# Kernel tuning notes

Hardware: AMD Instinct MI355X
Metric: run time of the kernel (lower is better)

The kernel has to match this reference:

```python
import jax, jax.numpy as jnp
import numpy as np

B, S = 2, 1024
HIDDEN = 2048
NUM_K, NUM_V = 16, 32
DK, DV = 128, 128
KCONV = 4
EPS = 1e-6
KEY_DIM = NUM_K * DK      # 2048
VAL_DIM = NUM_V * DV      # 4096
RATIO = NUM_V // NUM_K    # 2


def setup_inputs() -> dict:
    key = jax.random.key(0)
    ks = jax.random.split(key, 8)
    sc = lambda k, shape, s=0.02: jax.random.normal(k, shape, jnp.float32) * s
    return {
        "hidden_states": jax.random.normal(ks[0], (B, S, HIDDEN), jnp.float32),
        "W_qkvz": sc(ks[1], (HIDDEN, 2 * KEY_DIM + 2 * VAL_DIM)),
        "W_ba": sc(ks[2], (HIDDEN, 2 * NUM_V)),
        "conv_weight": sc(ks[3], (2 * KEY_DIM + VAL_DIM, KCONV), 0.1),
        "A_log": jnp.log(jax.random.uniform(ks[4], (NUM_V,), jnp.float32, 0.001, 16.0)),
        "dt_bias": jnp.ones((NUM_V,), jnp.float32),
        "norm_weight": jnp.ones((DV,), jnp.float32),
        "W_out": sc(ks[5], (VAL_DIM, HIDDEN)),
    }


def _l2norm(x):
    return x * jax.lax.rsqrt(jnp.sum(x * x, axis=-1, keepdims=True) + 1e-6)


def reference(hidden_states, W_qkvz, W_ba, conv_weight, A_log, dt_bias, norm_weight, W_out):
    Bb, Ss, _ = hidden_states.shape
    # fused in_proj + fix_query_key_value_ordering: per k-head layout [q|k|ratio*v|ratio*z]
    qkvz = (hidden_states @ W_qkvz).reshape(Bb, Ss, NUM_K, 2 * DK + 2 * RATIO * DV)
    q = qkvz[..., :DK]                                        # [B,S,NUM_K,DK]
    k = qkvz[..., DK:2 * DK]
    v = qkvz[..., 2 * DK:2 * DK + RATIO * DV].reshape(Bb, Ss, NUM_V, DV)
    z = qkvz[..., 2 * DK + RATIO * DV:].reshape(Bb, Ss, NUM_V, DV)
    ba = (hidden_states @ W_ba).reshape(Bb, Ss, NUM_K, 2 * RATIO)
    b = ba[..., :RATIO].reshape(Bb, Ss, NUM_V)
    a = ba[..., RATIO:].reshape(Bb, Ss, NUM_V)
    # causal depthwise conv over mixed qkv channels + silu (causal_conv1d)
    mixed = jnp.concatenate(
        [q.reshape(Bb, Ss, -1), k.reshape(Bb, Ss, -1), v.reshape(Bb, Ss, -1)], axis=-1)
    x = jnp.transpose(mixed, (0, 2, 1))                       # [B,C,S]
    x = jnp.pad(x, ((0, 0), (0, 0), (KCONV - 1, 0)))
    conv = jax.lax.conv_general_dilated(
        x, conv_weight[:, None, :], (1,), 'VALID',
        feature_group_count=x.shape[1],
        dimension_numbers=('NCH', 'OIH', 'NCH'))
    mixed = jax.nn.silu(jnp.transpose(conv, (0, 2, 1)))       # [B,S,conv_dim]
    q = mixed[..., :KEY_DIM].reshape(Bb, Ss, NUM_K, DK)
    k = mixed[..., KEY_DIM:2 * KEY_DIM].reshape(Bb, Ss, NUM_K, DK)
    v = mixed[..., 2 * KEY_DIM:].reshape(Bb, Ss, NUM_V, DV)
    # GQA: repeat each k-head to its RATIO consecutive v-heads
    q = jnp.repeat(q, RATIO, axis=2)
    k = jnp.repeat(k, RATIO, axis=2)
    q = _l2norm(q) * (DK ** -0.5)
    k = _l2norm(k)
    # fused_gdn_gating: g = -exp(A_log) * softplus(a + dt_bias); beta = sigmoid(b)
    g = -jnp.exp(A_log) * jax.nn.softplus(a + dt_bias)        # [B,S,H] fp32
    beta = jax.nn.sigmoid(b)
    # recurrent gated delta rule scan; state [B,H,DK,DV]
    def step(state, inp):
        qt, kt, vt, gt, bt = inp
        state = state * jnp.exp(gt)[..., None, None]
        pred = jnp.einsum('bhk,bhkv->bhv', kt, state)
        delta = (vt - pred) * bt[..., None]
        state = state + kt[..., None] * delta[..., None, :]
        out = jnp.einsum('bhk,bhkv->bhv', qt, state)
        return state, out

    xs = (q.transpose(1, 0, 2, 3), k.transpose(1, 0, 2, 3), v.transpose(1, 0, 2, 3),
          g.transpose(1, 0, 2), beta.transpose(1, 0, 2))
    state0 = jnp.zeros((Bb, NUM_V, DK, DV), jnp.float32)
    _, core = jax.lax.scan(step, state0, xs)                  # [S,B,H,DV]
    core = core.transpose(1, 0, 2, 3)
    # RMSNormGated (norm_before_gate=True): rmsnorm(x) * w * silu(z)
    var = jnp.mean(core * core, axis=-1, keepdims=True)
    core = core * jax.lax.rsqrt(var + EPS) * norm_weight * jax.nn.silu(z)
    return core.reshape(Bb, Ss, VAL_DIM) @ W_out              # [B,S,HIDDEN]
```

## Files before the change

### kernel.cpp

```cpp
#include <hip/hip_runtime.h>
#include <stdint.h>

#define B_ 2
#define S_ 1024
#define HID 2048
#define NK 16
#define NV 32
#define DK_ 128
#define DV_ 128
#define QKVZ_N 12288
#define TOK (B_*S_)
#define KROW 144

typedef unsigned short u16;
typedef __bf16 bf16x8 __attribute__((ext_vector_type(8)));
typedef float f32x4 __attribute__((ext_vector_type(4)));
typedef float f32x2 __attribute__((ext_vector_type(2)));
typedef unsigned short u16x8 __attribute__((ext_vector_type(8)));
typedef unsigned short u16x4 __attribute__((ext_vector_type(4)));

__device__ __forceinline__ float bf2f(u16 u) {
    return __builtin_bit_cast(float, (unsigned)u << 16);
}
__device__ __forceinline__ u16 f2bf(float f) {
    unsigned u = __builtin_bit_cast(unsigned, f);
    u += 0x7fff + ((u >> 16) & 1);
    return (u16)(u >> 16);
}

template <int CTRL>
__device__ __forceinline__ float dpp_add(float x) {
    int yi = __builtin_amdgcn_update_dpp(0, __builtin_bit_cast(int, x), CTRL, 0xF, 0xF, true);
    return x + __builtin_bit_cast(float, yi);
}
__device__ __forceinline__ float sum16(float x) {
    x = dpp_add<0xB1>(x);
    x = dpp_add<0x4E>(x);
    x = dpp_add<0x141>(x);
    x = dpp_add<0x140>(x);
    return x;
}

__device__ __forceinline__ void gl16(const void* g, void* l) {
    __builtin_amdgcn_global_load_lds((const __attribute__((address_space(1))) uint32_t*)g,
                                     (__attribute__((address_space(3))) uint32_t*)l, 16, 0, 0);
}
__device__ __forceinline__ void gl4(const void* g, void* l) {
    __builtin_amdgcn_global_load_lds((const __attribute__((address_space(1))) uint32_t*)g,
                                     (__attribute__((address_space(3))) uint32_t*)l, 4, 0, 0);
}

__global__ void k_cvt_bf16(const float* __restrict__ in, u16* __restrict__ out, int n) {
    int i = (blockIdx.x * blockDim.x + threadIdx.x) * 4;
    if (i >= n) return;
    float4 v = *(const float4*)(in + i);
    u16x4 o = { f2bf(v.x), f2bf(v.y), f2bf(v.z), f2bf(v.w) };
    *(u16x4*)(out + i) = o;
}

__global__ void k_transpose(const float* __restrict__ in, u16* __restrict__ out, int R, int C) {
    __shared__ float tile[32][33];
    int c0 = blockIdx.x * 32, r0 = blockIdx.y * 32;
    int tx = threadIdx.x, ty = threadIdx.y;
#pragma unroll
    for (int i = 0; i < 4; i++)
        tile[ty + i * 8][tx] = in[(size_t)(r0 + ty + i * 8) * C + c0 + tx];
    __syncthreads();
#pragma unroll
    for (int i = 0; i < 4; i++)
        out[(size_t)(c0 + ty + i * 8) * R + r0 + tx] = f2bf(tile[tx][ty + i * 8]);
}

template <int OUT_BF16>
__global__ __launch_bounds__(256) void k_gemm(const u16* __restrict__ A, const u16* __restrict__ Bt,
                                              void* __restrict__ Cv, int K, int ldc) {
    __shared__ u16 As[128 * 40];
    __shared__ u16 Bs[128 * 40];
    int tid = threadIdx.x;
    int bm = blockIdx.y, bn = blockIdx.x;
    int wid = tid >> 6, lane = tid & 63;
    int wm = wid >> 1, wn = wid & 1;
    int l15 = lane & 15, lg = lane >> 4;
    int srow = tid >> 2, schunk = (tid & 3) * 8;
    const u16* Ag = A + (size_t)(bm * 128 + srow) * K + schunk;
    const u16* Bg = Bt + (size_t)(bn * 128 + srow) * K + schunk;
    f32x4 acc[4][4] = {};
    for (int k0 = 0; k0 < K; k0 += 32) {
        u16x8 a0 = *(const u16x8*)(Ag + k0);
        u16x8 a1 = *(const u16x8*)(Ag + (size_t)64 * K + k0);
        u16x8 b0 = *(const u16x8*)(Bg + k0);
        u16x8 b1 = *(const u16x8*)(Bg + (size_t)64 * K + k0);
        __syncthreads();
        *(u16x8*)&As[srow * 40 + schunk] = a0;
        *(u16x8*)&As[(srow + 64) * 40 + schunk] = a1;
        *(u16x8*)&Bs[srow * 40 + schunk] = b0;
        *(u16x8*)&Bs[(srow + 64) * 40 + schunk] = b1;
        __syncthreads();
        bf16x8 af[4], bf[4];
#pragma unroll
        for (int mi = 0; mi < 4; mi++)
            af[mi] = __builtin_bit_cast(bf16x8, *(const u16x8*)&As[(wm * 64 + mi * 16 + l15) * 40 + lg * 8]);
#pragma unroll
        for (int ni = 0; ni < 4; ni++)
            bf[ni] = __builtin_bit_cast(bf16x8, *(const u16x8*)&Bs[(wn * 64 + ni * 16 + l15) * 40 + lg * 8]);
#pragma unroll
        for (int mi = 0; mi < 4; mi++)
#pragma unroll
            for (int ni = 0; ni < 4; ni++)
                acc[mi][ni] = __builtin_amdgcn_mfma_f32_16x16x32_bf16(af[mi], bf[ni], acc[mi][ni], 0, 0, 0);
    }
#pragma unroll
    for (int mi = 0; mi < 4; mi++) {
        int gr0 = bm * 128 + wm * 64 + mi * 16 + lg * 4;
#pragma unroll
        for (int ni = 0; ni < 4; ni++) {
            int gc = bn * 128 + wn * 64 + ni * 16 + l15;
#pragma unroll
            for (int r = 0; r < 4; r++) {
                if (OUT_BF16)
                    ((u16*)Cv)[(size_t)(gr0 + r) * ldc + gc] = f2bf(acc[mi][ni][r]);
                else
                    ((float*)Cv)[(size_t)(gr0 + r) * ldc + gc] = acc[mi][ni][r];
            }
        }
    }
}

__global__ void k_ba(const float* __restrict__ hid, const float* __restrict__ Wba, float* __restrict__ ba) {
    int token = blockIdx.x;
    int c = threadIdx.x;
    const float* h = hid + (size_t)token * HID;
    const float* w = Wba + c;
    float acc = 0.f;
    for (int k = 0; k < HID; k += 4) {
        float4 hv = *(const float4*)(h + k);
        acc += hv.x * w[(size_t)k * 64] + hv.y * w[(size_t)(k + 1) * 64] +
               hv.z * w[(size_t)(k + 2) * 64] + hv.w * w[(size_t)(k + 3) * 64];
    }
    ba[(size_t)token * 64 + c] = acc;
}

__global__ __launch_bounds__(256) void k_conv(const u16* __restrict__ qkvz, const float* __restrict__ ba,
                                              const float* __restrict__ cw, const float* __restrict__ A_log,
                                              const float* __restrict__ dt_bias, float* __restrict__ qs,
                                              float* __restrict__ ks, float* __restrict__ vs,
                                              float2* __restrict__ gb2) {
    __shared__ float sm[4096];
    int token = blockIdx.x;
    int b = token >> 10;
    int t = token & (S_ - 1);
    int tid = threadIdx.x;
    const u16* row3 = qkvz + (size_t)token * QKVZ_N;
#pragma unroll
    for (int i = 0; i < 32; i++) {
        int c = tid + i * 256;
        int col;
        if (c < 2048) col = (c >> 7) * 768 + (c & 127);
        else if (c < 4096) col = ((c - 2048) >> 7) * 768 + 128 + (c & 127);
        else {
            int cc = c - 4096;
            col = (cc >> 8) * 768 + 256 + ((cc >> 7) & 1) * 128 + (cc & 127);
        }
        float4 w = *(const float4*)(cw + c * 4);
        float x3 = bf2f(row3[col]);
        float x2 = (t >= 1) ? bf2f(row3[col - QKVZ_N]) : 0.f;
        float x1 = (t >= 2) ? bf2f(row3[col - 2 * QKVZ_N]) : 0.f;
        float x0 = (t >= 3) ? bf2f(row3[col - 3 * QKVZ_N]) : 0.f;
        float s = w.x * x0 + w.y * x1 + w.z * x2 + w.w * x3;
        s = s / (1.f + __expf(-s));
        if (c < 4096) sm[c] = s;
        else {
            int cc = c - 4096;
            int hv = cc >> 7, d = cc & 127;
            vs[((size_t)(b * NV + hv) * S_ + t) * 128 + d] = s;
        }
    }
    __syncthreads();
    int grp = tid >> 3, l8 = tid & 7;
    float vals[16];
    float ss = 0.f;
    const float* sp = sm + grp * 128 + l8 * 16;
#pragma unroll
    for (int i = 0; i < 16; i++) { vals[i] = sp[i]; ss += vals[i] * vals[i]; }
    ss += __shfl_xor(ss, 1); ss += __shfl_xor(ss, 2); ss += __shfl_xor(ss, 4);
    float scale = rsqrtf(ss + 1e-6f);
    if (grp < 16) scale *= 0.08838834764831845f;
    float* op = (grp < 16 ? qs : ks) + ((size_t)(b * NK + (grp & 15)) * S_ + t) * KROW
              + l8 * 16 + (l8 >> 1) * 4;
#pragma unroll
    for (int i = 0; i < 16; i++) op[i] = vals[i] * scale;
    if (tid < 32) {
        int hv = tid;
        float bval = ba[(size_t)token * 64 + (hv >> 1) * 4 + (hv & 1)];
        float aval = ba[(size_t)token * 64 + (hv >> 1) * 4 + 2 + (hv & 1)];
        float x = aval + dt_bias[hv];
        float sp2 = (x > 20.f) ? x : log1pf(__expf(x));
        float eg = __expf(-__expf(A_log[hv]) * sp2);
        float bt = 1.f / (1.f + __expf(-bval));
        gb2[(size_t)(b * NV + hv) * S_ + t] = make_float2(eg, bt);
    }
}

__global__ __launch_bounds__(512) void k_scan(const float* __restrict__ qs, const float* __restrict__ ks,
                                              const float* __restrict__ vs, const float2* __restrict__ gb2,
                                              float* __restrict__ core) {
    __shared__ float kb[2][32 * KROW];
    __shared__ float qb[2][32 * KROW];
    __shared__ float vbf[2][32 * 32];
    __shared__ float2 gbl[2][32];
    int bid = blockIdx.x;
    int bh = bid >> 2, vsp = bid & 3;
    int b = bh >> 5, hv = bh & 31, hk = hv >> 1;
    int tid = threadIdx.x;
    int wid = tid >> 6, lane = tid & 63;
    int vloc = tid >> 4, rq = tid & 15;
    const char* kgb = (const char*)(ks + (size_t)(b * NK + hk) * S_ * KROW);
    const char* qgb = (const char*)(qs + (size_t)(b * NK + hk) * S_ * KROW);
    const char* vgb = (const char*)(vs + ((size_t)(b * NV + hv) * S_) * 128 + vsp * 32);
    const char* ggb = (const char*)(gb2 + (size_t)(b * NV + hv) * S_);
    float* cp = core + ((size_t)(b * NV + hv) * S_) * 128 + vsp * 32 + vloc;
    bool writer = (rq == 0);
    int koff = rq * 8 + (rq >> 2) * 4;

    auto stage = [&](int tile, int buf) {
        const char* kg = kgb + (size_t)tile * 32 * (KROW * 4);
        const char* qg = qgb + (size_t)tile * 32 * (KROW * 4);
        const char* vg = vgb + (size_t)tile * 32 * 512;
        const char* gg = ggb + (size_t)tile * 32 * 8;
        for (int ch = wid; ch < 41; ch += 8) {
            if (ch < 18)
                gl16(kg + ch * 1024 + lane * 16, (char*)&kb[buf][0] + ch * 1024);
            else if (ch < 36)
                gl16(qg + (ch - 18) * 1024 + lane * 16, (char*)&qb[buf][0] + (ch - 18) * 1024);
            else if (ch < 40) {
                int c4 = ch - 36;
                gl16(vg + (size_t)(c4 * 8 + (lane >> 3)) * 512 + (lane & 7) * 16,
                     (char*)&vbf[buf][0] + c4 * 1024);
            } else
                gl4(gg + lane * 4, (char*)&gbl[buf][0]);
        }
    };

    f32x2 st2[4] = {};
    stage(0, 0);
    __syncthreads();
    for (int tile = 0; tile < 32; ++tile) {
        int buf = tile & 1;
        if (tile < 31) stage(tile + 1, buf ^ 1);
        const float* kT = &kb[buf][0];
        const float* qT = &qb[buf][0];
        const float* vT = &vbf[buf][0];
        const float2* gT = &gbl[buf][0];
#pragma unroll
        for (int t = 0; t < 32; ++t) {
            f32x4 kA = *(const f32x4*)(kT + t * KROW + koff);
            f32x4 kB = *(const f32x4*)(kT + t * KROW + koff + 4);
            f32x4 qA = *(const f32x4*)(qT + t * KROW + koff);
            f32x4 qB = *(const f32x4*)(qT + t * KROW + koff + 4);
            float vv = vT[t * 32 + vloc];
            float2 gv = gT[t];
            f32x2 k0 = __builtin_shufflevector(kA, kA, 0, 1);
            f32x2 k1 = __builtin_shufflevector(kA, kA, 2, 3);
            f32x2 k2 = __builtin_shufflevector(kB, kB, 0, 1);
            f32x2 k3 = __builtin_shufflevector(kB, kB, 2, 3);
            f32x2 p0 = k0 * st2[0];
            p0 = __builtin_elementwise_fma(k1, st2[1], p0);
            f32x2 p1 = k2 * st2[2];
            p1 = __builtin_elementwise_fma(k3, st2[3], p1);
            f32x2 ps = p0 + p1;
            float dks = sum16(ps.x + ps.y);
            float eg = gv.x;
            float delta = (vv - eg * dks) * gv.y;
            f32x2 e2 = {eg, eg}, d2 = {delta, delta};
            st2[0] = __builtin_elementwise_fma(st2[0], e2, k0 * d2);
            st2[1] = __builtin_elementwise_fma(st2[1], e2, k1 * d2);
            st2[2] = __builtin_elementwise_fma(st2[2], e2, k2 * d2);
            st2[3] = __builtin_elementwise_fma(st2[3], e2, k3 * d2);
            f32x2 q0 = __builtin_shufflevector(qA, qA, 0, 1);
            f32x2 q1 = __builtin_shufflevector(qA, qA, 2, 3);
            f32x2 q2 = __builtin_shufflevector(qB, qB, 0, 1);
            f32x2 q3 = __builtin_shufflevector(qB, qB, 2, 3);
            f32x2 o0 = q0 * st2[0];
            o0 = __builtin_elementwise_fma(q1, st2[1], o0);
            f32x2 o1 = q2 * st2[2];
            o1 = __builtin_elementwise_fma(q3, st2[3], o1);
            f32x2 os = o0 + o1;
            float dqs = sum16(os.x + os.y);
            if (writer) cp[(size_t)(tile * 32 + t) * 128] = dqs;
        }
        __syncthreads();
    }
}

__global__ __launch_bounds__(256) void k_gate(const float* __restrict__ core, const u16* __restrict__ qkvz,
                                              const float* __restrict__ nw, u16* __restrict__ gated) {
    int token = blockIdx.x, tid = threadIdx.x;
    int b = token >> 10, t = token & (S_ - 1);
    int grp = tid >> 3, l8 = tid & 7;
    const float* cp = core + ((size_t)(b * NV + grp) * S_ + t) * DV_ + l8 * 16;
    float vals[16];
    float ss = 0.f;
#pragma unroll
    for (int i = 0; i < 16; i++) { vals[i] = cp[i]; ss += vals[i] * vals[i]; }
    ss += __shfl_xor(ss, 1); ss += __shfl_xor(ss, 2); ss += __shfl_xor(ss, 4);
    float rms = rsqrtf(ss * (1.0f / DV_) + 1e-6f);
    const u16* zp = qkvz + (size_t)token * QKVZ_N + (grp >> 1) * 768 + 512 + (grp & 1) * 128 + l8 * 16;
    u16* op = gated + ((size_t)token * NV + grp) * DV_ + l8 * 16;
#pragma unroll
    for (int i = 0; i < 16; i++) {
        float z = bf2f(zp[i]);
        float sz = z / (1.f + __expf(-z));
        op[i] = f2bf(vals[i] * rms * nw[l8 * 16 + i] * sz);
    }
}

extern "C" void kernel_launch(void* const* d_in, const int* in_sizes, int n_in,
                              void* d_out, int out_size, void* d_ws, size_t ws_size,
                              hipStream_t stream) {
    const float* hidden = (const float*)d_in[0];
    const float* Wqkvz = (const float*)d_in[1];
    const float* Wba = (const float*)d_in[2];
    const float* convw = (const float*)d_in[3];
    const float* A_log = (const float*)d_in[4];
    const float* dt_bias = (const float*)d_in[5];
    const float* norm_w = (const float*)d_in[6];
    const float* Wout = (const float*)d_in[7];

    char* ws = (char*)d_ws;
    size_t off = 0;
    auto alloc = [&](size_t bytes) -> void* {
        void* p = ws + off;
        off += (bytes + 255) & ~(size_t)255;
        return p;
    };
    u16* hiddenB = (u16*)alloc((size_t)TOK * HID * 2);
    u16* WqT = (u16*)alloc((size_t)QKVZ_N * HID * 2);
    u16* WoT = (u16*)alloc((size_t)HID * 4096 * 2);
    u16* qkvz = (u16*)alloc((size_t)TOK * QKVZ_N * 2);
    float* ba = (float*)alloc((size_t)TOK * 64 * 4);
    float* qs = (float*)alloc((size_t)B_ * NK * S_ * KROW * 4);
    float* ks = (float*)alloc((size_t)B_ * NK * S_ * KROW * 4);
    float* vs = (float*)alloc((size_t)B_ * NV * S_ * 128 * 4);
    float2* gb2 = (float2*)alloc((size_t)B_ * NV * S_ * 8);
    float* core = (float*)alloc((size_t)B_ * NV * S_ * 128 * 4);
    u16* gated = (u16*)alloc((size_t)TOK * 4096 * 2);

    k_cvt_bf16<<<4096, 256, 0, stream>>>(hidden, hiddenB, TOK * HID);
    k_transpose<<<dim3(QKVZ_N / 32, HID / 32), dim3(32, 8), 0, stream>>>(Wqkvz, WqT, HID, QKVZ_N);
    k_transpose<<<dim3(HID / 32, 4096 / 32), dim3(32, 8), 0, stream>>>(Wout, WoT, 4096, HID);
    k_gemm<1><<<dim3(QKVZ_N / 128, TOK / 128), 256, 0, stream>>>(hiddenB, WqT, qkvz, HID, QKVZ_N);
    k_ba<<<TOK, 64, 0, stream>>>(hidden, Wba, ba);
    k_conv<<<TOK, 256, 0, stream>>>(qkvz, ba, convw, A_log, dt_bias, qs, ks, vs, gb2);
    k_scan<<<256, 512, 0, stream>>>(qs, ks, vs, gb2, core);
    k_gate<<<TOK, 256, 0, stream>>>(core, qkvz, norm_w, gated);
    k_gemm<0><<<dim3(HID / 128, TOK / 128), 256, 0, stream>>>(gated, WoT, d_out, 4096, HID);
}
```

Baseline: 647.3 us.

## Repad q/k rows, force packed FMA asm, stage scan outputs in LDS

Changes the padded q/k row layout from 144 to 160 floats, with each 8-float group at a stride of 10 floats, to alter LDS bank mapping for the per-lane 2-float loads in the scan kernel. The producer kernel writes q/k with vector stores to match. The recurrence math now uses inline v_pk_mul_f32/v_pk_fma_f32 asm so packed FP32 instructions are guaranteed. Per-step outputs are buffered in a double-buffered LDS tile and written to global memory as coalesced 2-float stores per tile, instead of scattered single-float stores from one lane in sixteen. The cost is more staging traffic and LDS from the wider padding.

Result: slower. 671.9 us (+3.8%).

```diff
diff --git a/kernel.cpp b/kernel.cpp
--- a/kernel.cpp
+++ b/kernel.cpp
@@ -10,7 +10,7 @@
 #define DV_ 128
 #define QKVZ_N 12288
 #define TOK (B_*S_)
-#define KROW 144
+#define KROW 160
 
 typedef unsigned short u16;
 typedef __bf16 bf16x8 __attribute__((ext_vector_type(8)));
@@ -39,6 +39,17 @@
     x = dpp_add<0x141>(x);
     x = dpp_add<0x140>(x);
     return x;
+}
+
+__device__ __forceinline__ f32x2 pk_mul(f32x2 a, f32x2 b) {
+    f32x2 d;
+    asm("v_pk_mul_f32 %0, %1, %2" : "=v"(d) : "v"(a), "v"(b));
+    return d;
+}
+__device__ __forceinline__ f32x2 pk_fma(f32x2 a, f32x2 b, f32x2 c) {
+    f32x2 d;
+    asm("v_pk_fma_f32 %0, %1, %2, %3" : "=v"(d) : "v"(a), "v"(b), "v"(c));
+    return d;
 }
 
 __device__ __forceinline__ void gl16(const void* g, void* l) {
@@ -185,10 +196,13 @@
     ss += __shfl_xor(ss, 1); ss += __shfl_xor(ss, 2); ss += __shfl_xor(ss, 4);
     float scale = rsqrtf(ss + 1e-6f);
     if (grp < 16) scale *= 0.08838834764831845f;
-    float* op = (grp < 16 ? qs : ks) + ((size_t)(b * NK + (grp & 15)) * S_ + t) * KROW
-              + l8 * 16 + (l8 >> 1) * 4;
-#pragma unroll
-    for (int i = 0; i < 16; i++) op[i] = vals[i] * scale;
+    float* op = (grp < 16 ? qs : ks) + ((size_t)(b * NK + (grp & 15)) * S_ + t) * KROW + 20 * l8;
+    *(float4*)(op)      = make_float4(vals[0]*scale, vals[1]*scale, vals[2]*scale, vals[3]*scale);
+    *(float4*)(op + 4)  = make_float4(vals[4]*scale, vals[5]*scale, vals[6]*scale, vals[7]*scale);
+    *(float2*)(op + 10) = make_float2(vals[8]*scale, vals[9]*scale);
+    *(float2*)(op + 12) = make_float2(vals[10]*scale, vals[11]*scale);
+    *(float2*)(op + 14) = make_float2(vals[12]*scale, vals[13]*scale);
+    *(float2*)(op + 16) = make_float2(vals[14]*scale, vals[15]*scale);
     if (tid < 32) {
         int hv = tid;
         float bval = ba[(size_t)token * 64 + (hv >> 1) * 4 + (hv & 1)];
@@ -208,6 +222,7 @@
     __shared__ float qb[2][32 * KROW];
     __shared__ float vbf[2][32 * 32];
     __shared__ float2 gbl[2][32];
+    __shared__ float outb[2][32 * 32];
     int bid = blockIdx.x;
     int bh = bid >> 2, vsp = bid & 3;
     int b = bh >> 5, hv = bh & 31, hk = hv >> 1;
@@ -218,26 +233,26 @@
     const char* qgb = (const char*)(qs + (size_t)(b * NK + hk) * S_ * KROW);
     const char* vgb = (const char*)(vs + ((size_t)(b * NV + hv) * S_) * 128 + vsp * 32);
     const char* ggb = (const char*)(gb2 + (size_t)(b * NV + hv) * S_);
-    float* cp = core + ((size_t)(b * NV + hv) * S_) * 128 + vsp * 32 + vloc;
+    float* cpb = core + ((size_t)(b * NV + hv) * S_) * 128 + vsp * 32;
     bool writer = (rq == 0);
-    int koff = rq * 8 + (rq >> 2) * 4;
-
-    auto stage = [&](int tile, int buf) {
-        const char* kg = kgb + (size_t)tile * 32 * (KROW * 4);
-        const char* qg = qgb + (size_t)tile * 32 * (KROW * 4);
+    int koff = 10 * rq;
+
+    auto stage = [&](int tile, int bufi) {
+        const char* kg = kgb + (size_t)tile * (32 * KROW * 4);
+        const char* qg = qgb + (size_t)tile * (32 * KROW * 4);
         const char* vg = vgb + (size_t)tile * 32 * 512;
-        const char* gg = ggb + (size_t)tile * 32 * 8;
-        for (int ch = wid; ch < 41; ch += 8) {
-            if (ch < 18)
-                gl16(kg + ch * 1024 + lane * 16, (char*)&kb[buf][0] + ch * 1024);
-            else if (ch < 36)
-                gl16(qg + (ch - 18) * 1024 + lane * 16, (char*)&qb[buf][0] + (ch - 18) * 1024);
-            else if (ch < 40) {
-                int c4 = ch - 36;
+        const char* gg = ggb + (size_t)tile * 256;
+        for (int ch = wid; ch < 45; ch += 8) {
+            if (ch < 20)
+                gl16(kg + ch * 1024 + lane * 16, (char*)&kb[bufi][0] + ch * 1024);
+            else if (ch < 40)
+                gl16(qg + (ch - 20) * 1024 + lane * 16, (char*)&qb[bufi][0] + (ch - 20) * 1024);
+            else if (ch < 44) {
+                int c4 = ch - 40;
                 gl16(vg + (size_t)(c4 * 8 + (lane >> 3)) * 512 + (lane & 7) * 16,
-                     (char*)&vbf[buf][0] + c4 * 1024);
+                     (char*)&vbf[bufi][0] + c4 * 1024);
             } else
-                gl4(gg + lane * 4, (char*)&gbl[buf][0]);
+                gl4(gg + lane * 4, (char*)&gbl[bufi][0]);
         }
     };
 
@@ -251,44 +266,42 @@
         const float* qT = &qb[buf][0];
         const float* vT = &vbf[buf][0];
         const float2* gT = &gbl[buf][0];
+        float* oT = &outb[buf][0];
 #pragma unroll
         for (int t = 0; t < 32; ++t) {
-            f32x4 kA = *(const f32x4*)(kT + t * KROW + koff);
-            f32x4 kB = *(const f32x4*)(kT + t * KROW + koff + 4);
-            f32x4 qA = *(const f32x4*)(qT + t * KROW + koff);
-            f32x4 qB = *(const f32x4*)(qT + t * KROW + koff + 4);
+            const float* kr = kT + t * KROW + koff;
+            const float* qr = qT + t * KROW + koff;
+            f32x2 k0 = *(const f32x2*)(kr);
+            f32x2 k1 = *(const f32x2*)(kr + 2);
+            f32x2 k2 = *(const f32x2*)(kr + 4);
+            f32x2 k3 = *(const f32x2*)(kr + 6);
+            f32x2 q0 = *(const f32x2*)(qr);
+            f32x2 q1 = *(const f32x2*)(qr + 2);
+            f32x2 q2 = *(const f32x2*)(qr + 4);
+            f32x2 q3 = *(const f32x2*)(qr + 6);
             float vv = vT[t * 32 + vloc];
             float2 gv = gT[t];
-            f32x2 k0 = __builtin_shufflevector(kA, kA, 0, 1);
-            f32x2 k1 = __builtin_shufflevector(kA, kA, 2, 3);
-            f32x2 k2 = __builtin_shufflevector(kB, kB, 0, 1);
-            f32x2 k3 = __builtin_shufflevector(kB, kB, 2, 3);
-            f32x2 p0 = k0 * st2[0];
-            p0 = __builtin_elementwise_fma(k1, st2[1], p0);
-            f32x2 p1 = k2 * st2[2];
-            p1 = __builtin_elementwise_fma(k3, st2[3], p1);
-            f32x2 ps = p0 + p1;
-            float dks = sum16(ps.x + ps.y);
-            float eg = gv.x;
-            float delta = (vv - eg * dks) * gv.y;
-            f32x2 e2 = {eg, eg}, d2 = {delta, delta};
-            st2[0] = __builtin_elementwise_fma(st2[0], e2, k0 * d2);
-            st2[1] = __builtin_elementwise_fma(st2[1], e2, k1 * d2);
-            st2[2] = __builtin_elementwise_fma(st2[2], e2, k2 * d2);
-            st2[3] = __builtin_elementwise_fma(st2[3], e2, k3 * d2);
-            f32x2 q0 = __builtin_shufflevector(qA, qA, 0, 1);
-            f32x2 q1 = __builtin_shufflevector(qA, qA, 2, 3);
-            f32x2 q2 = __builtin_shufflevector(qB, qB, 0, 1);
-            f32x2 q3 = __builtin_shufflevector(qB, qB, 2, 3);
-            f32x2 o0 = q0 * st2[0];
-            o0 = __builtin_elementwise_fma(q1, st2[1], o0);
-            f32x2 o1 = q2 * st2[2];
-            o1 = __builtin_elementwise_fma(q3, st2[3], o1);
-            f32x2 os = o0 + o1;
-            float dqs = sum16(os.x + os.y);
-            if (writer) cp[(size_t)(tile * 32 + t) * 128] = dqs;
+            f32x2 pa = pk_fma(k1, st2[1], pk_mul(k0, st2[0]));
+            f32x2 pb = pk_fma(k3, st2[3], pk_mul(k2, st2[2]));
+            float dks = sum16((pa.x + pb.x) + (pa.y + pb.y));
+            float delta = (vv - gv.x * dks) * gv.y;
+            f32x2 e2; e2.x = gv.x; e2.y = gv.x;
+            f32x2 d2; d2.x = delta; d2.y = delta;
+            st2[0] = pk_fma(st2[0], e2, pk_mul(k0, d2));
+            st2[1] = pk_fma(st2[1], e2, pk_mul(k1, d2));
+            st2[2] = pk_fma(st2[2], e2, pk_mul(k2, d2));
+            st2[3] = pk_fma(st2[3], e2, pk_mul(k3, d2));
+            f32x2 oa = pk_fma(q1, st2[1], pk_mul(q0, st2[0]));
+            f32x2 ob = pk_fma(q3, st2[3], pk_mul(q2, st2[2]));
+            float dqs = sum16((oa.x + ob.x) + (oa.y + ob.y));
+            if (writer) oT[t * 32 + vloc] = dqs;
         }
         __syncthreads();
+        {
+            int trow = tid >> 4, c2 = (tid & 15) * 2;
+            f32x2 val = *(const f32x2*)&outb[buf][trow * 32 + c2];
+            *(f32x2*)(cpb + (size_t)(tile * 32 + trow) * 128 + c2) = val;
+        }
     }
 }
 
```

## Use direct global-to-LDS loads in GEMM, repad q/k rows, stage scan outputs

Applied to the files above, without the earlier changes.

The GEMM now loads its A and B tiles straight into unpadded LDS with gl16 direct-to-LDS copies, split by wave, instead of going through registers with padded stores. The q/k row stride changes from 144 to 192 floats with a 12-float-per-lane offset pattern, and the prep kernel writes those rows with float4 stores. The scan kernel collects per-timestep outputs in a double-buffered LDS tile and writes them out as coalesced float2 stores after each tile, replacing scattered single-float global writes. The trade-offs are larger LDS and global footprint for q/k, possible bank conflicts from the unpadded GEMM tiles, and extra LDS traffic in the scan.

New measurement: 612.5 us. -5.4%, faster.

```diff
diff --git a/kernel.cpp b/kernel.cpp
--- a/kernel.cpp
+++ b/kernel.cpp
@@ -10,7 +10,7 @@
 #define DV_ 128
 #define QKVZ_N 12288
 #define TOK (B_*S_)
-#define KROW 144
+#define KROW 192
 
 typedef unsigned short u16;
 typedef __bf16 bf16x8 __attribute__((ext_vector_type(8)));
@@ -74,35 +74,33 @@
 template <int OUT_BF16>
 __global__ __launch_bounds__(256) void k_gemm(const u16* __restrict__ A, const u16* __restrict__ Bt,
                                               void* __restrict__ Cv, int K, int ldc) {
-    __shared__ u16 As[128 * 40];
-    __shared__ u16 Bs[128 * 40];
+    __shared__ u16 As[128 * 32];
+    __shared__ u16 Bs[128 * 32];
     int tid = threadIdx.x;
     int bm = blockIdx.y, bn = blockIdx.x;
     int wid = tid >> 6, lane = tid & 63;
     int wm = wid >> 1, wn = wid & 1;
     int l15 = lane & 15, lg = lane >> 4;
-    int srow = tid >> 2, schunk = (tid & 3) * 8;
-    const u16* Ag = A + (size_t)(bm * 128 + srow) * K + schunk;
-    const u16* Bg = Bt + (size_t)(bn * 128 + srow) * K + schunk;
+    const u16* src0 = (wid >> 1) ? (Bt + (size_t)bn * 128 * K) : (A + (size_t)bm * 128 * K);
+    u16* ldsb = (wid >> 1) ? Bs : As;
+    int cbase = (wid & 1) * 4;
+    int lrow = lane >> 2, lcol = (lane & 3) * 8;
     f32x4 acc[4][4] = {};
     for (int k0 = 0; k0 < K; k0 += 32) {
-        u16x8 a0 = *(const u16x8*)(Ag + k0);
-        u16x8 a1 = *(const u16x8*)(Ag + (size_t)64 * K + k0);
-        u16x8 b0 = *(const u16x8*)(Bg + k0);
-        u16x8 b1 = *(const u16x8*)(Bg + (size_t)64 * K + k0);
-        __syncthreads();
-        *(u16x8*)&As[srow * 40 + schunk] = a0;
-        *(u16x8*)&As[(srow + 64) * 40 + schunk] = a1;
-        *(u16x8*)&Bs[srow * 40 + schunk] = b0;
-        *(u16x8*)&Bs[(srow + 64) * 40 + schunk] = b1;
+        if (k0) __syncthreads();
+#pragma unroll
+        for (int c = 0; c < 4; c++) {
+            int ch = cbase + c;
+            gl16(src0 + (size_t)(16 * ch + lrow) * K + k0 + lcol, (char*)ldsb + ch * 1024);
+        }
         __syncthreads();
         bf16x8 af[4], bf[4];
 #pragma unroll
         for (int mi = 0; mi < 4; mi++)
-            af[mi] = __builtin_bit_cast(bf16x8, *(const u16x8*)&As[(wm * 64 + mi * 16 + l15) * 40 + lg * 8]);
+            af[mi] = __builtin_bit_cast(bf16x8, *(const u16x8*)&As[(wm * 64 + mi * 16 + l15) * 32 + lg * 8]);
 #pragma unroll
         for (int ni = 0; ni < 4; ni++)
-            bf[ni] = __builtin_bit_cast(bf16x8, *(const u16x8*)&Bs[(wn * 64 + ni * 16 + l15) * 40 + lg * 8]);
+            bf[ni] = __builtin_bit_cast(bf16x8, *(const u16x8*)&Bs[(wn * 64 + ni * 16 + l15) * 32 + lg * 8]);
 #pragma unroll
         for (int mi = 0; mi < 4; mi++)
 #pragma unroll
@@ -185,10 +183,11 @@
     ss += __shfl_xor(ss, 1); ss += __shfl_xor(ss, 2); ss += __shfl_xor(ss, 4);
     float scale = rsqrtf(ss + 1e-6f);
     if (grp < 16) scale *= 0.08838834764831845f;
-    float* op = (grp < 16 ? qs : ks) + ((size_t)(b * NK + (grp & 15)) * S_ + t) * KROW
-              + l8 * 16 + (l8 >> 1) * 4;
-#pragma unroll
-    for (int i = 0; i < 16; i++) op[i] = vals[i] * scale;
+    float* op = (grp < 16 ? qs : ks) + ((size_t)(b * NK + (grp & 15)) * S_ + t) * KROW + 24 * l8;
+    *(float4*)(op)      = make_float4(vals[0]*scale, vals[1]*scale, vals[2]*scale, vals[3]*scale);
+    *(float4*)(op + 4)  = make_float4(vals[4]*scale, vals[5]*scale, vals[6]*scale, vals[7]*scale);
+    *(float4*)(op + 12) = make_float4(vals[8]*scale, vals[9]*scale, vals[10]*scale, vals[11]*scale);
+    *(float4*)(op + 16) = make_float4(vals[12]*scale, vals[13]*scale, vals[14]*scale, vals[15]*scale);
     if (tid < 32) {
         int hv = tid;
         float bval = ba[(size_t)token * 64 + (hv >> 1) * 4 + (hv & 1)];
@@ -208,6 +207,7 @@
     __shared__ float qb[2][32 * KROW];
     __shared__ float vbf[2][32 * 32];
     __shared__ float2 gbl[2][32];
+    __shared__ float outb[2][32 * 32];
     int bid = blockIdx.x;
     int bh = bid >> 2, vsp = bid & 3;
     int b = bh >> 5, hv = bh & 31, hk = hv >> 1;
@@ -218,26 +218,26 @@
     const char* qgb = (const char*)(qs + (size_t)(b * NK + hk) * S_ * KROW);
     const char* vgb = (const char*)(vs + ((size_t)(b * NV + hv) * S_) * 128 + vsp * 32);
     const char* ggb = (const char*)(gb2 + (size_t)(b * NV + hv) * S_);
-    float* cp = core + ((size_t)(b * NV + hv) * S_) * 128 + vsp * 32 + vloc;
+    float* cpb = core + ((size_t)(b * NV + hv) * S_) * 128 + vsp * 32;
     bool writer = (rq == 0);
-    int koff = rq * 8 + (rq >> 2) * 4;
-
-    auto stage = [&](int tile, int buf) {
-        const char* kg = kgb + (size_t)tile * 32 * (KROW * 4);
-        const char* qg = qgb + (size_t)tile * 32 * (KROW * 4);
+    int koff = 12 * rq;
+
+    auto stage = [&](int tile, int bufi) {
+        const char* kg = kgb + (size_t)tile * (32 * KROW * 4);
+        const char* qg = qgb + (size_t)tile * (32 * KROW * 4);
         const char* vg = vgb + (size_t)tile * 32 * 512;
-        const char* gg = ggb + (size_t)tile * 32 * 8;
-        for (int ch = wid; ch < 41; ch += 8) {
-            if (ch < 18)
-                gl16(kg + ch * 1024 + lane * 16, (char*)&kb[buf][0] + ch * 1024);
-            else if (ch < 36)
-                gl16(qg + (ch - 18) * 1024 + lane * 16, (char*)&qb[buf][0] + (ch - 18) * 1024);
-            else if (ch < 40) {
-                int c4 = ch - 36;
+        const char* gg = ggb + (size_t)tile * 256;
+        for (int ch = wid; ch < 53; ch += 8) {
+            if (ch < 24)
+                gl16(kg + ch * 1024 + lane * 16, (char*)&kb[bufi][0] + ch * 1024);
+            else if (ch < 48)
+                gl16(qg + (ch - 24) * 1024 + lane * 16, (char*)&qb[bufi][0] + (ch - 24) * 1024);
+            else if (ch < 52) {
+                int c4 = ch - 48;
                 gl16(vg + (size_t)(c4 * 8 + (lane >> 3)) * 512 + (lane & 7) * 16,
-                     (char*)&vbf[buf][0] + c4 * 1024);
+                     (char*)&vbf[bufi][0] + c4 * 1024);
             } else
-                gl4(gg + lane * 4, (char*)&gbl[buf][0]);
+                gl4(gg + lane * 4, (char*)&gbl[bufi][0]);
         }
     };
 
@@ -251,6 +251,7 @@
         const float* qT = &qb[buf][0];
         const float* vT = &vbf[buf][0];
         const float2* gT = &gbl[buf][0];
+        float* oT = &outb[buf][0];
 #pragma unroll
         for (int t = 0; t < 32; ++t) {
             f32x4 kA = *(const f32x4*)(kT + t * KROW + koff);
@@ -263,12 +264,9 @@
             f32x2 k1 = __builtin_shufflevector(kA, kA, 2, 3);
             f32x2 k2 = __builtin_shufflevector(kB, kB, 0, 1);
             f32x2 k3 = __builtin_shufflevector(kB, kB, 2, 3);
-            f32x2 p0 = k0 * st2[0];
-            p0 = __builtin_elementwise_fma(k1, st2[1], p0);
-            f32x2 p1 = k2 * st2[2];
-            p1 = __builtin_elementwise_fma(k3, st2[3], p1);
-            f32x2 ps = p0 + p1;
-            float dks = sum16(ps.x + ps.y);
+            f32x2 pa = __builtin_elementwise_fma(k1, st2[1], k0 * st2[0]);
+            f32x2 pb = __builtin_elementwise_fma(k3, st2[3], k2 * st2[2]);
+            float dks = sum16((pa.x + pb.x) + (pa.y + pb.y));
             float eg = gv.x;
             float delta = (vv - eg * dks) * gv.y;
             f32x2 e2 = {eg, eg}, d2 = {delta, delta};
@@ -280,15 +278,17 @@
             f32x2 q1 = __builtin_shufflevector(qA, qA, 2, 3);
             f32x2 q2 = __builtin_shufflevector(qB, qB, 0, 1);
             f32x2 q3 = __builtin_shufflevector(qB, qB, 2, 3);
-            f32x2 o0 = q0 * st2[0];
-            o0 = __builtin_elementwise_fma(q1, st2[1], o0);
-            f32x2 o1 = q2 * st2[2];
-            o1 = __builtin_elementwise_fma(q3, st2[3], o1);
-            f32x2 os = o0 + o1;
-            float dqs = sum16(os.x + os.y);
-            if (writer) cp[(size_t)(tile * 32 + t) * 128] = dqs;
+            f32x2 oa = __builtin_elementwise_fma(q1, st2[1], q0 * st2[0]);
+            f32x2 ob = __builtin_elementwise_fma(q3, st2[3], q2 * st2[2]);
+            float dqs = sum16((oa.x + ob.x) + (oa.y + ob.y));
+            if (writer) oT[t * 32 + vloc] = dqs;
         }
         __syncthreads();
+        {
+            int trow = tid >> 4, c2 = (tid & 15) * 2;
+            f32x2 val = *(const f32x2*)&outb[buf][trow * 32 + c2];
+            *(f32x2*)(cpb + (size_t)(tile * 32 + trow) * 128 + c2) = val;
+        }
     }
 }
 
```
